# Optimization experiments

Hardware: AMD Instinct MI355X
Metric: run time of the kernel (lower is better)

The kernel has to match this reference:

```python
import jax, jax.numpy as jnp
import numpy as np

B, S, D = 8, 2048, 1024

def setup_inputs() -> dict:
    key = jax.random.key(0)
    ks = jax.random.split(key, 7)
    x = jax.random.normal(ks[0], (B, S, D), dtype=jnp.float32)
    s = 1.0 / np.sqrt(D)
    Wq = jax.random.normal(ks[1], (D, D), dtype=jnp.float32) * s
    bq = jax.random.normal(ks[2], (D,), dtype=jnp.float32) * 0.01
    Wk = jax.random.normal(ks[3], (D, D), dtype=jnp.float32) * s
    bk = jax.random.normal(ks[4], (D,), dtype=jnp.float32) * 0.01
    Wv = jax.random.normal(ks[5], (D, D), dtype=jnp.float32) * s
    bv = jax.random.normal(ks[6], (D,), dtype=jnp.float32) * 0.01
    return {"x": x, "Wq": Wq, "bq": bq, "Wk": Wk, "bk": bk, "Wv": Wv, "bv": bv}

def reference(x, Wq, bq, Wk, bk, Wv, bv):
    # QKV projections: [B,S,D]
    Q = jnp.einsum('bsd,de->bse', x, Wq) + bq
    K = jnp.einsum('bsd,de->bse', x, Wk) + bk
    V = jnp.einsum('bsd,de->bse', x, Wv) + bv
    scale = 1.0 / jnp.sqrt(jnp.asarray(Q.shape[-1], Q.dtype))
    attn = jnp.einsum('bqd,bkd->bqk', Q, K) * scale  # [B,S,S]
    attn = jax.nn.softmax(attn, axis=-1)
    return jnp.einsum('bqk,bkd->bqd', attn, V)
```

## Files before the change

kernel.cpp:

```cpp
#include <hip/hip_runtime.h>
#include <cstdint>


#define Bb 8
#define Ss 2048
#define Dd 1024

typedef unsigned short ushort_t;
typedef __attribute__((ext_vector_type(8))) short short8;
typedef __attribute__((ext_vector_type(4))) float floatx4;

__device__ inline ushort_t f2bf(float f) {
    unsigned int u = __float_as_uint(f);
    unsigned int r = (u + 0x7fffu + ((u >> 16) & 1u)) >> 16;
    return (ushort_t)r;
}
__device__ inline float bf2f(ushort_t u) {
    return __uint_as_float(((unsigned int)u) << 16);
}

__device__ inline floatx4 mfma16(short8 a, short8 b, floatx4 c) {
    return __builtin_amdgcn_mfma_f32_16x16x32_bf16(a, b, c, 0, 0, 0);
}

__device__ inline void gload16(const void* g, void* l) {
    __builtin_amdgcn_global_load_lds(
        (const __attribute__((address_space(1))) void*)g,
        (__attribute__((address_space(3))) void*)l, 16, 0, 0);
}

__device__ __attribute__((always_inline)) void gemm_core256(
    const ushort_t* __restrict__ A, const ushort_t* __restrict__ B,
    int K, int lda, int ldb, int m0, int n0, int tid,
    ushort_t* lds, floatx4 acc[8][4])
{
    const int lane = tid & 63;
    const int wave = tid >> 6;
    const int l3   = lane >> 3;
    const int kc   = ((lane & 7) ^ l3) * 8;

    const ushort_t* aS[2][2];
    const ushort_t* bS[2][2];
#pragma unroll
    for (int i = 0; i < 2; i++) {
#pragma unroll
        for (int g = 0; g < 2; g++) {
            const int r = i * 128 + g * 64 + wave * 8 + l3;
            aS[g][i] = A + (size_t)(m0 + r) * lda + kc;
        }
#pragma unroll
        for (int nh = 0; nh < 2; nh++) {
            const int c = wave + i * 8;
            const int r = (c >> 2) * 64 + nh * 32 + (c & 3) * 8 + l3;
            bS[nh][i] = B + (size_t)(n0 + r) * ldb + kc;
        }
    }

    const int jA   = (wave >> 2) * 64 + (lane & 15);
    const int jB   = (wave & 3) * 32 + (lane & 15);
    const int swz0 = (((lane >> 4) + 0) ^ (lane & 7)) * 8;
    const int swz1 = (((lane >> 4) + 4) ^ (lane & 7)) * 8;

    short8 aF[4][2], bF[2][2];

#define STG(DST, REGI, SRC, KOFS)                                             \
    do {                                                                      \
        gload16(SRC[0] + (KOFS), (DST) + (REGI) * 8192 + wave * 512);         \
        gload16(SRC[1] + (KOFS), (DST) + (REGI) * 8192 + (wave + 8) * 512);   \
    } while (0)

#define RD_A(QM)                                                              \
    _Pragma("unroll")                                                         \
    for (int mi = 0; mi < 4; mi++) {                                          \
        const ushort_t* pA_ = cb + (QM) * 8192 + (jA + mi * 16) * 64;         \
        aF[mi][0] = *(const short8*)&pA_[swz0];                               \
        aF[mi][1] = *(const short8*)&pA_[swz1];                               \
    }

#define RD_B(QN)                                                              \
    _Pragma("unroll")                                                         \
    for (int ni = 0; ni < 2; ni++) {                                          \
        const ushort_t* pB_ = cb + (2 + (QN)) * 8192 + (jB + ni * 16) * 64;   \
        bF[ni][0] = *(const short8*)&pB_[swz0];                               \
        bF[ni][1] = *(const short8*)&pB_[swz1];                               \
    }

#define MM(QM, QN)                                                            \
    _Pragma("unroll")                                                         \
    for (int ks = 0; ks < 2; ks++)                                            \
        _Pragma("unroll")                                                     \
        for (int mi = 0; mi < 4; mi++)                                        \
            _Pragma("unroll")                                                 \
            for (int ni = 0; ni < 2; ni++)                                    \
                acc[(QM) * 4 + mi][(QN) * 2 + ni] =                           \
                    mfma16(aF[mi][ks], bF[ni][ks],                            \
                           acc[(QM) * 4 + mi][(QN) * 2 + ni]);

#define PHASE(RDS, MMS, STGS, VMS)                                            \
    do {                                                                      \
        RDS                                                                   \
        STGS;                                                                 \
        __builtin_amdgcn_sched_barrier(0);                                    \
        __builtin_amdgcn_s_barrier();                                         \
        asm volatile("s_waitcnt lgkmcnt(0)" ::: "memory");                    \
        __builtin_amdgcn_sched_barrier(0);                                    \
        __builtin_amdgcn_s_setprio(1);                                        \
        MMS                                                                   \
        __builtin_amdgcn_s_setprio(0);                                        \
        __builtin_amdgcn_sched_barrier(0);                                    \
        VMS;                                                                  \
        __builtin_amdgcn_s_barrier();                                         \
        __builtin_amdgcn_sched_barrier(0);                                    \
    } while (0)

    STG(lds, 0, aS[0], 0);
    STG(lds, 1, aS[1], 0);
    STG(lds, 2, bS[0], 0);
    STG(lds, 3, bS[1], 0);
    STG(lds + 32768, 2, bS[0], 64);
    STG(lds + 32768, 1, aS[1], 64);
    asm volatile("s_waitcnt vmcnt(4)" ::: "memory");
    __builtin_amdgcn_s_barrier();
    __builtin_amdgcn_sched_barrier(0);

    const int NT = K >> 6;
    for (int t = 0; t < NT; t++) {
        const ushort_t* cb = lds + (t & 1) * 32768;
        ushort_t* nb = lds + ((t + 1) & 1) * 32768;
        ushort_t* sb = lds + (t & 1) * 32768;
        const int k1 = (t + 1 < NT ? t + 1 : 0) << 6;
        const int k2 = (t + 2 < NT ? t + 2 : 0) << 6;
        PHASE(RD_A(0) RD_B(0), MM(0, 0), STG(nb, 3, bS[1], k1), (void)0);
        PHASE(RD_A(1),         MM(1, 0), STG(nb, 0, aS[0], k1), (void)0);
        PHASE(RD_B(1),         MM(1, 1), STG(sb, 2, bS[0], k2), (void)0);
        PHASE(RD_A(0),         MM(0, 1), STG(sb, 1, aS[1], k2),
              asm volatile("s_waitcnt vmcnt(4)" ::: "memory"));
    }
    asm volatile("s_waitcnt vmcnt(0)" ::: "memory");
#undef PHASE
#undef MM
#undef RD_B
#undef RD_A
#undef STG
}

template <int EPI>
__global__ __launch_bounds__(512, 2) void gemm256(
    const ushort_t* __restrict__ A, const ushort_t* __restrict__ B,
    void* __restrict__ Cv, float* __restrict__ aux,
    int K, int lda, int ldb, int ldc,
    size_t strideA, size_t strideB, size_t strideC)
{
    const int z = blockIdx.z;
    A += (size_t)z * strideA;
    B += (size_t)z * strideB;
    const int m0 = blockIdx.y * 256;
    const int n0 = blockIdx.x * 256;

    __shared__ __align__(16) ushort_t lds[2 * 4 * 8192];

    floatx4 acc[8][4] = {};
    gemm_core256(A, B, K, lda, ldb, m0, n0, (int)threadIdx.x, lds, acc);

    const int lane = threadIdx.x & 63;
    const int wave = threadIdx.x >> 6;
    const int row0 = m0 + (wave >> 2) * 128 + (lane >> 4) * 4;
    const int col0 = n0 + (wave & 3) * 64 + (lane & 15);

    if (EPI == 0) {
        ushort_t* Cb = (ushort_t*)Cv;
        float bval[4];
#pragma unroll
        for (int nf = 0; nf < 4; nf++) bval[nf] = aux[col0 + nf * 16];
#pragma unroll
        for (int mf = 0; mf < 8; mf++)
#pragma unroll
            for (int i = 0; i < 4; i++) {
                const size_t ro = (size_t)(row0 + mf * 16 + i) * ldc;
#pragma unroll
                for (int nf = 0; nf < 4; nf++)
                    Cb[ro + col0 + nf * 16] = f2bf(acc[mf][nf][i] + bval[nf]);
            }
    } else if (EPI == 1) {
        ushort_t* Cb = (ushort_t*)Cv + (size_t)z * strideC;
        float* ls = aux + z * Ss;
        float rs[8][4];
#pragma unroll
        for (int mf = 0; mf < 8; mf++)
#pragma unroll
            for (int i = 0; i < 4; i++) rs[mf][i] = 0.f;
#pragma unroll
        for (int mf = 0; mf < 8; mf++)
#pragma unroll
            for (int i = 0; i < 4; i++) {
                const size_t ro = (size_t)(row0 + mf * 16 + i) * ldc;
#pragma unroll
                for (int nf = 0; nf < 4; nf++) {
                    const ushort_t o = f2bf(__expf(acc[mf][nf][i] * 0.03125f));
                    Cb[ro + col0 + nf * 16] = o;
                    rs[mf][i] += bf2f(o);
                }
            }
#pragma unroll
        for (int mf = 0; mf < 8; mf++)
#pragma unroll
            for (int i = 0; i < 4; i++) {
                float s = rs[mf][i];
                s += __shfl_xor(s, 1);
                s += __shfl_xor(s, 2);
                s += __shfl_xor(s, 4);
                s += __shfl_xor(s, 8);
                rs[mf][i] = s;
            }
        if ((lane & 15) == 0) {
#pragma unroll
            for (int mf = 0; mf < 8; mf++)
#pragma unroll
                for (int i = 0; i < 4; i++)
                    atomicAdd(&ls[row0 + mf * 16 + i], rs[mf][i]);
        }
    } else {
        float* Cf = (float*)Cv + (size_t)z * strideC;
#pragma unroll
        for (int mf = 0; mf < 8; mf++)
#pragma unroll
            for (int i = 0; i < 4; i++) {
                const int gr = row0 + mf * 16 + i;
                const float iv = 1.0f / aux[z * Ss + gr];
#pragma unroll
                for (int nf = 0; nf < 4; nf++)
                    Cf[(size_t)gr * ldc + col0 + nf * 16] = acc[mf][nf][i] * iv;
            }
    }
}

__global__ __launch_bounds__(256) void vtrans(
    const ushort_t* __restrict__ QKVb, ushort_t* __restrict__ Vt)
{
    __shared__ __align__(16) ushort_t tile[64][72];
    const int t = blockIdx.x;
    const int z = t >> 9, rem = t & 511;
    const int d0 = (rem & 15) * 64, s0 = (rem >> 4) * 64;
    const int tid = threadIdx.x;
    const int rr = tid >> 3;
    const int c8 = (tid & 7) * 8;
#pragma unroll
    for (int i = 0; i < 2; i++) {
        const int s = s0 + rr + i * 32;
        uint4 v = *(const uint4*)&QKVb[((size_t)(z * Ss + s)) * 3072 + 2048 + d0 + c8];
        *(uint4*)&tile[rr + i * 32][c8] = v;
    }
    __syncthreads();
#pragma unroll
    for (int i = 0; i < 2; i++) {
        const int d = rr + i * 32;
        ushort_t u[8];
#pragma unroll
        for (int j = 0; j < 8; j++) u[j] = tile[c8 + j][d];
        *(uint4*)&Vt[(size_t)z * Dd * Ss + (size_t)(d0 + d) * Ss + s0 + c8] =
            *(const uint4*)u;
    }
}

__global__ __launch_bounds__(256) void prep(
    const float* __restrict__ x,
    const float* __restrict__ W0, const float* __restrict__ W1,
    const float* __restrict__ W2,
    const float* __restrict__ bq, const float* __restrict__ bk,
    const float* __restrict__ bv,
    ushort_t* __restrict__ xb, ushort_t* __restrict__ Wall,
    float* __restrict__ ball)
{
    const int bid = blockIdx.x;
    const int tid = threadIdx.x;

    if (bid < 8192) {
        const size_t i = (size_t)bid * 256 + tid;
        const float4* p = (const float4*)x + i * 2;
        float4 a = p[0], b = p[1];
        ushort_t u[8];
        u[0]=f2bf(a.x); u[1]=f2bf(a.y); u[2]=f2bf(a.z); u[3]=f2bf(a.w);
        u[4]=f2bf(b.x); u[5]=f2bf(b.y); u[6]=f2bf(b.z); u[7]=f2bf(b.w);
        *(uint4*)(xb + i * 8) = *(const uint4*)u;
    } else if (bid < 8960) {
        const int t = bid - 8192;
        const int z = t >> 8;
        const float* W = (z == 0) ? W0 : (z == 1) ? W1 : W2;
        ushort_t* Wt = Wall + (size_t)z * Dd * Dd;
        __shared__ float tt[64][65];
        const int n0 = ((t >> 4) & 15) * 64, k0 = (t & 15) * 64;
        const int r  = tid >> 4;
        const int c4 = (tid & 15) * 4;
#pragma unroll
        for (int i = 0; i < 4; i++) {
            float4 v = *(const float4*)&W[(size_t)(k0 + r + i * 16) * Dd + n0 + c4];
            tt[r + i * 16][c4 + 0] = v.x;
            tt[r + i * 16][c4 + 1] = v.y;
            tt[r + i * 16][c4 + 2] = v.z;
            tt[r + i * 16][c4 + 3] = v.w;
        }
        __syncthreads();
#pragma unroll
        for (int i = 0; i < 4; i++) {
            const int rn = r + i * 16;
            ushort_t u[4];
#pragma unroll
            for (int j = 0; j < 4; j++) u[j] = f2bf(tt[c4 + j][rn]);
            *(uint2*)&Wt[(size_t)(n0 + rn) * Dd + k0 + c4] = *(const uint2*)u;
        }
    } else {
#pragma unroll
        for (int j = 0; j < 12; j++) {
            const int idx = j * 256 + tid;
            float v = (idx < 1024) ? bq[idx]
                    : (idx < 2048) ? bk[idx - 1024] : bv[idx - 2048];
            ball[idx] = v;
        }
    }
}

extern "C" void kernel_launch(void* const* d_in, const int* in_sizes, int n_in,
                              void* d_out, int out_size, void* d_ws, size_t ws_size,
                              hipStream_t stream)
{
    const float* x  = (const float*)d_in[0];
    const float* Wq = (const float*)d_in[1];
    const float* bq = (const float*)d_in[2];
    const float* Wk = (const float*)d_in[3];
    const float* bk = (const float*)d_in[4];
    const float* Wv = (const float*)d_in[5];
    const float* bv = (const float*)d_in[6];
    float* out = (float*)d_out;

    char* ws = (char*)d_ws;
    const size_t MB = 1u << 20;
    ushort_t* xb   = (ushort_t*)(ws);
    ushort_t* Vt   = (ushort_t*)(ws);
    ushort_t* QKVb = (ushort_t*)(ws + 32 * MB);
    ushort_t* Pb   = (ushort_t*)(ws + 128 * MB);
    float*    lsum = (float*)(ws + 192 * MB);
    ushort_t* Wall = (ushort_t*)d_out;
    float*    ball = (float*)((char*)d_out + 6 * MB);

    prep<<<8961, 256, 0, stream>>>(x, Wq, Wk, Wv, bq, bk, bv, xb, Wall, ball);

    dim3 g1(3072 / 256, 16384 / 256, 1);
    gemm256<0><<<g1, 512, 0, stream>>>(xb, Wall, QKVb, ball,
                                       Dd, Dd, Dd, 3072, 0, 0, 0);

    hipMemsetAsync(lsum, 0, (size_t)Bb * Ss * sizeof(float), stream);
    vtrans<<<4096, 256, 0, stream>>>(QKVb, Vt);
    dim3 g2(Ss / 256, Ss / 256, Bb);
    gemm256<1><<<g2, 512, 0, stream>>>(QKVb, QKVb + 1024, Pb, lsum,
                                       Dd, 3072, 3072, Ss,
                                       (size_t)Ss * 3072, (size_t)Ss * 3072,
                                       (size_t)Ss * Ss);

    dim3 g3(Dd / 256, Ss / 256, Bb);
    gemm256<3><<<g3, 512, 0, stream>>>(Pb, Vt, out, lsum,
                                       Ss, Ss, Ss, Dd,
                                       (size_t)Ss * Ss, (size_t)Dd * Ss,
                                       (size_t)Ss * Dd);
}
```

Measured before the change: 398.2 us.

## Restructure GEMM main loop: load all B fragments once, double-buffer A fragments

New measurement: 372.4 us. 1.07x faster.

```diff
diff --git a/kernel.cpp b/kernel.cpp
--- a/kernel.cpp
+++ b/kernel.cpp
@@ -61,7 +61,8 @@
     const int swz0 = (((lane >> 4) + 0) ^ (lane & 7)) * 8;
     const int swz1 = (((lane >> 4) + 4) ^ (lane & 7)) * 8;
 
-    short8 aF[4][2], bF[2][2];
+    short8 bFr[4][2];
+    short8 aE[2][2], aO[2][2];
 
 #define STG(DST, REGI, SRC, KOFS)                                             \
     do {                                                                      \
@@ -69,47 +70,41 @@
         gload16(SRC[1] + (KOFS), (DST) + (REGI) * 8192 + (wave + 8) * 512);   \
     } while (0)
 
-#define RD_A(QM)                                                              \
+#define RD_B_ALL(BUF)                                                         \
     _Pragma("unroll")                                                         \
-    for (int mi = 0; mi < 4; mi++) {                                          \
-        const ushort_t* pA_ = cb + (QM) * 8192 + (jA + mi * 16) * 64;         \
-        aF[mi][0] = *(const short8*)&pA_[swz0];                               \
-        aF[mi][1] = *(const short8*)&pA_[swz1];                               \
-    }
-
-#define RD_B(QN)                                                              \
+    for (int nf = 0; nf < 4; nf++) {                                          \
+        const ushort_t* pB_ =                                                 \
+            (BUF) + (2 + (nf >> 1)) * 8192 + (jB + (nf & 1) * 16) * 64;       \
+        bFr[nf][0] = *(const short8*)&pB_[swz0];                              \
+        bFr[nf][1] = *(const short8*)&pB_[swz1];                              \
+    }
+
+#define RD_A(BUF, Q, DST)                                                     \
     _Pragma("unroll")                                                         \
-    for (int ni = 0; ni < 2; ni++) {                                          \
-        const ushort_t* pB_ = cb + (2 + (QN)) * 8192 + (jB + ni * 16) * 64;   \
-        bF[ni][0] = *(const short8*)&pB_[swz0];                               \
-        bF[ni][1] = *(const short8*)&pB_[swz1];                               \
-    }
-
-#define MM(QM, QN)                                                            \
+    for (int mi = 0; mi < 2; mi++) {                                          \
+        const ushort_t* pA_ = (BUF) + ((Q) >> 1) * 8192 +                     \
+                              (jA + ((Q) & 1) * 32 + mi * 16) * 64;           \
+        DST[mi][0] = *(const short8*)&pA_[swz0];                              \
+        DST[mi][1] = *(const short8*)&pA_[swz1];                              \
+    }
+
+#define MM(Q, ASRC)                                                           \
     _Pragma("unroll")                                                         \
     for (int ks = 0; ks < 2; ks++)                                            \
         _Pragma("unroll")                                                     \
-        for (int mi = 0; mi < 4; mi++)                                        \
+        for (int mi = 0; mi < 2; mi++)                                        \
             _Pragma("unroll")                                                 \
-            for (int ni = 0; ni < 2; ni++)                                    \
-                acc[(QM) * 4 + mi][(QN) * 2 + ni] =                           \
-                    mfma16(aF[mi][ks], bF[ni][ks],                            \
-                           acc[(QM) * 4 + mi][(QN) * 2 + ni]);
-
-#define PHASE(RDS, MMS, STGS, VMS)                                            \
+            for (int nf = 0; nf < 4; nf++)                                    \
+                acc[(Q) * 2 + mi][nf] =                                       \
+                    mfma16(ASRC[mi][ks], bFr[nf][ks], acc[(Q) * 2 + mi][nf]);
+
+#define MMPH(Q, ASRC)                                                         \
     do {                                                                      \
-        RDS                                                                   \
-        STGS;                                                                 \
-        __builtin_amdgcn_sched_barrier(0);                                    \
-        __builtin_amdgcn_s_barrier();                                         \
         asm volatile("s_waitcnt lgkmcnt(0)" ::: "memory");                    \
         __builtin_amdgcn_sched_barrier(0);                                    \
         __builtin_amdgcn_s_setprio(1);                                        \
-        MMS                                                                   \
+        MM(Q, ASRC);                                                          \
         __builtin_amdgcn_s_setprio(0);                                        \
-        __builtin_amdgcn_sched_barrier(0);                                    \
-        VMS;                                                                  \
-        __builtin_amdgcn_s_barrier();                                         \
         __builtin_amdgcn_sched_barrier(0);                                    \
     } while (0)
 
@@ -118,7 +113,7 @@
     STG(lds, 2, bS[0], 0);
     STG(lds, 3, bS[1], 0);
     STG(lds + 32768, 2, bS[0], 64);
-    STG(lds + 32768, 1, aS[1], 64);
+    STG(lds + 32768, 3, bS[1], 64);
     asm volatile("s_waitcnt vmcnt(4)" ::: "memory");
     __builtin_amdgcn_s_barrier();
     __builtin_amdgcn_sched_barrier(0);
@@ -130,17 +125,34 @@
         ushort_t* sb = lds + (t & 1) * 32768;
         const int k1 = (t + 1 < NT ? t + 1 : 0) << 6;
         const int k2 = (t + 2 < NT ? t + 2 : 0) << 6;
-        PHASE(RD_A(0) RD_B(0), MM(0, 0), STG(nb, 3, bS[1], k1), (void)0);
-        PHASE(RD_A(1),         MM(1, 0), STG(nb, 0, aS[0], k1), (void)0);
-        PHASE(RD_B(1),         MM(1, 1), STG(sb, 2, bS[0], k2), (void)0);
-        PHASE(RD_A(0),         MM(0, 1), STG(sb, 1, aS[1], k2),
-              asm volatile("s_waitcnt vmcnt(4)" ::: "memory"));
+
+        RD_B_ALL(cb);
+        RD_A(cb, 0, aE);
+
+        MMPH(0, aE);
+        RD_A(cb, 1, aO);
+        STG(nb, 0, aS[0], k1);
+        MMPH(1, aO);
+        RD_A(cb, 2, aE);
+        STG(nb, 1, aS[1], k1);
+        __builtin_amdgcn_sched_barrier(0);
+        __builtin_amdgcn_s_barrier();
+        __builtin_amdgcn_sched_barrier(0);
+        MMPH(2, aE);
+        RD_A(cb, 3, aO);
+        STG(sb, 2, bS[0], k2);
+        MMPH(3, aO);
+        STG(sb, 3, bS[1], k2);
+        __builtin_amdgcn_sched_barrier(0);
+        asm volatile("s_waitcnt vmcnt(4)" ::: "memory");
+        __builtin_amdgcn_s_barrier();
+        __builtin_amdgcn_sched_barrier(0);
     }
     asm volatile("s_waitcnt vmcnt(0)" ::: "memory");
-#undef PHASE
+#undef MMPH
 #undef MM
-#undef RD_B
 #undef RD_A
+#undef RD_B_ALL
 #undef STG
 }
 
```
